# Performance work log

Hardware: AMD Instinct MI355X
Metric: run time of the kernel (lower is better)

The kernel has to match this reference:

```python
import jax, jax.numpy as jnp
import numpy as np

D_MODEL = 1024
N_HEAD = 16
D_HEAD = D_MODEL // N_HEAD
NEG = -1e9


def setup_inputs() -> dict:
    key = jax.random.key(0)
    ks = jax.random.split(key, 11)
    B, T, C = 4, 2048, D_MODEL
    s = 1.0 / np.sqrt(C)
    return {
        "q": jax.random.normal(ks[0], (B, T, C), jnp.float32),
        "k": jax.random.normal(ks[1], (B, T, C), jnp.float32),
        "v": jax.random.normal(ks[2], (B, T, C), jnp.float32),
        "w_q": jax.random.normal(ks[3], (C, C), jnp.float32) * s,
        "b_q": jnp.zeros((C,), jnp.float32),
        "w_k": jax.random.normal(ks[4], (C, C), jnp.float32) * s,
        "b_k": jnp.zeros((C,), jnp.float32),
        "w_v": jax.random.normal(ks[5], (C, C), jnp.float32) * s,
        "b_v": jnp.zeros((C,), jnp.float32),
        "w_o": jax.random.normal(ks[6], (C, C), jnp.float32) * s,
        "b_o": jnp.zeros((C,), jnp.float32),
    }


def reference(q, k, v, w_q, b_q, w_k, b_k, w_v, b_v, w_o, b_o):
    B, T, C = q.shape
    # projections; weights stored as [in, out]
    qh = (q @ w_q + b_q).reshape(B, T, N_HEAD, D_HEAD).transpose(0, 2, 1, 3)
    kh = (k @ w_k + b_k).reshape(B, T, N_HEAD, D_HEAD).transpose(0, 2, 1, 3)
    vh = (v @ w_v + b_v).reshape(B, T, N_HEAD, D_HEAD).transpose(0, 2, 1, 3)
    scores = jnp.einsum("bhqd,bhkd->bhqk", qh, kh) / jnp.sqrt(
        jnp.asarray(D_HEAD, qh.dtype))
    causal = jnp.tril(jnp.ones((T, T), dtype=bool))  # [T,T]
    scores = jnp.where(causal[None, None], scores, NEG)
    attn = jax.nn.softmax(scores, axis=-1)
    out = jnp.einsum("bhqk,bhkd->bhqd", attn, vh)
    out = out.transpose(0, 2, 1, 3).reshape(B, T, C)
    return out @ w_o + b_o
```

## Files before the change

kernel.cpp:

```cpp
#include <hip/hip_runtime.h>
#include <hip/hip_bf16.h>
#include <cstdint>
#include <cstddef>

#define DEVI static __device__ __forceinline__

typedef __attribute__((ext_vector_type(8))) short short8;
typedef __attribute__((ext_vector_type(4))) float f32x4;

typedef __attribute__((address_space(1))) const unsigned int as1c_uint;
typedef __attribute__((address_space(3))) unsigned int as3_uint;

constexpr int Bn = 4, Tn = 2048, Cn = 1024, Hn = 16, Dn = 64;
constexpr int Mtot = Bn * Tn;
#define QSCALE (0.125f * 1.44269504088896340736f)

DEVI unsigned short f2bf(float f) {
  unsigned u = __float_as_uint(f);
  u += 0x7fffu + ((u >> 16) & 1u);
  return (unsigned short)(u >> 16);
}
DEVI unsigned short f2bf_t(float f) {
  return (unsigned short)(__float_as_uint(f) >> 16);
}

DEVI void async16(const void* g, void* l) {
  __builtin_amdgcn_global_load_lds((as1c_uint*)g, (as3_uint*)l, 16, 0, 0);
}

__global__ __launch_bounds__(256) void transpose_cvt4(
    const float* __restrict__ w0, const float* __restrict__ w1,
    const float* __restrict__ w2, const float* __restrict__ w3,
    unsigned short* __restrict__ o0, unsigned short* __restrict__ o1,
    unsigned short* __restrict__ o2, unsigned short* __restrict__ o3) {
  __shared__ float tile[32][33];
  const int z = blockIdx.z;
  const float* w = z == 0 ? w0 : z == 1 ? w1 : z == 2 ? w2 : w3;
  unsigned short* wT = z == 0 ? o0 : z == 1 ? o1 : z == 2 ? o2 : o3;
  int n0 = blockIdx.x * 32, k0 = blockIdx.y * 32;
  int tx = threadIdx.x, ty = threadIdx.y;
#pragma unroll
  for (int r = 0; r < 32; r += 8)
    tile[ty + r][tx] = w[(size_t)(k0 + ty + r) * Cn + n0 + tx];
  __syncthreads();
  const int t = ty * 32 + tx;
  const int n_l = t >> 3;
  const int kq = (t & 7) * 4;
  const int n = n0 + n_l, k = k0 + kq;
  ushort4 pk;
#pragma unroll
  for (int e = 0; e < 4; ++e) ((unsigned short*)&pk)[e] = f2bf(tile[kq + e][n_l]);
  size_t idx = (size_t)((((n >> 4) * 32 + (k >> 5)) * 64 + ((k >> 3) & 3) * 16 + (n & 15))) * 8 + (k & 7);
  *(ushort4*)&wT[idx] = pk;
}

DEVI short8 xfrag(const unsigned short* Xlds, int i, int kc, int l15, int l4) {
  int row = i * 16 + l15;
  return *(const short8*)&Xlds[row * 1024 + (((kc * 4 + l4) ^ (row & 7)) * 8)];
}

template <int IB, int NJ, bool SWAP>
DEVI void proj_core(const unsigned short* __restrict__ wF,
                    const unsigned short* Xlds, int njb, int lane,
                    f32x4 (&acc)[IB][NJ]) {
  const int l15 = lane & 15, l4 = lane >> 4;
  const short8* wp = (const short8*)wF;
  short8 wfA[NJ], wfB[NJ];
#pragma unroll
  for (int j = 0; j < NJ; ++j) wfA[j] = wp[(size_t)((njb + j) * 32) * 64 + lane];
#pragma unroll 1
  for (int kc = 0; kc < 32; kc += 2) {
#pragma unroll
    for (int j = 0; j < NJ; ++j)
      wfB[j] = wp[(size_t)((njb + j) * 32 + kc + 1) * 64 + lane];
    short8 xf[IB];
#pragma unroll
    for (int i = 0; i < IB; ++i) xf[i] = xfrag(Xlds, i, kc, l15, l4);
#pragma unroll
    for (int i = 0; i < IB; ++i)
#pragma unroll
      for (int j = 0; j < NJ; ++j)
        acc[i][j] = SWAP
            ? __builtin_amdgcn_mfma_f32_16x16x32_bf16(xf[i], wfA[j], acc[i][j], 0, 0, 0)
            : __builtin_amdgcn_mfma_f32_16x16x32_bf16(wfA[j], xf[i], acc[i][j], 0, 0, 0);
    if (kc + 2 < 32) {
#pragma unroll
      for (int j = 0; j < NJ; ++j)
        wfA[j] = wp[(size_t)((njb + j) * 32 + kc + 2) * 64 + lane];
    }
#pragma unroll
    for (int i = 0; i < IB; ++i) xf[i] = xfrag(Xlds, i, kc + 1, l15, l4);
#pragma unroll
    for (int i = 0; i < IB; ++i)
#pragma unroll
      for (int j = 0; j < NJ; ++j)
        acc[i][j] = SWAP
            ? __builtin_amdgcn_mfma_f32_16x16x32_bf16(xf[i], wfB[j], acc[i][j], 0, 0, 0)
            : __builtin_amdgcn_mfma_f32_16x16x32_bf16(wfB[j], xf[i], acc[i][j], 0, 0, 0);
  }
}

DEVI void stage64_f32(const float* __restrict__ src, int m0,
                      unsigned short* Xlds, int tid) {
#pragma unroll
  for (int it = 0; it < 8; ++it) {
    int g = it * 1024 + tid;
    int row = g >> 7, slot = g & 127;
    const float4* p = (const float4*)(src + (size_t)(m0 + row) * Cn + slot * 8);
    float4 a = p[0], b = p[1];
    short8 sv;
    sv[0] = (short)f2bf(a.x); sv[1] = (short)f2bf(a.y);
    sv[2] = (short)f2bf(a.z); sv[3] = (short)f2bf(a.w);
    sv[4] = (short)f2bf(b.x); sv[5] = (short)f2bf(b.y);
    sv[6] = (short)f2bf(b.z); sv[7] = (short)f2bf(b.w);
    *(short8*)&Xlds[row * 1024 + ((slot ^ (row & 7)) * 8)] = sv;
  }
}

DEVI void stage32_bf(const unsigned short* __restrict__ src, int m0,
                     unsigned short* Xlds, int tid) {
#pragma unroll
  for (int it = 0; it < 8; ++it) {
    int s = it * 512 + tid;
    int row = s >> 7, sl = s & 127;
    async16(src + (size_t)(m0 + row) * Cn + ((sl ^ (row & 7)) * 8),
            Xlds + (size_t)(it * 512 + (tid & ~63)) * 8);
  }
}

__global__ __launch_bounds__(1024, 4) void proj_qkv(
    const float* __restrict__ xqf, const float* __restrict__ xkf,
    const float* __restrict__ xvf, const unsigned short* __restrict__ wFq,
    const unsigned short* __restrict__ wFk, const unsigned short* __restrict__ wFv,
    const float* __restrict__ bq, const float* __restrict__ bk,
    const float* __restrict__ bv, unsigned short* __restrict__ oq,
    unsigned short* __restrict__ ok, unsigned short* __restrict__ ov) {
  __shared__ unsigned short Xlds[64 * 1024];
  const int tid = threadIdx.x, lane = tid & 63, w = tid >> 6;
  const int l15 = lane & 15, l4 = lane >> 4;
  const int bid = blockIdx.x;
  const int z = bid >> 8;
  const int r = bid & 255;
  const int m0 = (r >> 1) * 64;
  const int nh = r & 1;
  const float* xz = z == 0 ? xqf : z == 1 ? xkf : xvf;
  const unsigned short* wF = z == 0 ? wFq : z == 1 ? wFk : wFv;
  const float* bias = z == 0 ? bq : z == 1 ? bk : bv;

  stage64_f32(xz, m0, Xlds, tid);
  __syncthreads();

  const f32x4 zf = {0.f, 0.f, 0.f, 0.f};
  f32x4 acc[4][2];
#pragma unroll
  for (int i = 0; i < 4; ++i)
#pragma unroll
    for (int j = 0; j < 2; ++j) acc[i][j] = zf;

  const int njb = nh * 32 + w * 2;
  if (z < 2)
    proj_core<4, 2, false>(wF, Xlds, njb, lane, acc);
  else
    proj_core<4, 2, true>(wF, Xlds, njb, lane, acc);

  const int b = m0 >> 11, t0loc = m0 & 2047;
  if (z < 2) {
    unsigned short* o = z == 0 ? oq : ok;
    const float scale = z == 0 ? QSCALE : 1.f;
#pragma unroll
    for (int j = 0; j < 2; ++j) {
      int ng = njb + j;
      int h = ng >> 2, d0 = (ng & 3) * 16 + l4 * 4;
      float4 bv4 = *(const float4*)&bias[ng * 16 + l4 * 4];
#pragma unroll
      for (int i = 0; i < 4; ++i) {
        int t = t0loc + i * 16 + l15;
        ushort4 pk;
        pk.x = f2bf((acc[i][j][0] + bv4.x) * scale);
        pk.y = f2bf((acc[i][j][1] + bv4.y) * scale);
        pk.z = f2bf((acc[i][j][2] + bv4.z) * scale);
        pk.w = f2bf((acc[i][j][3] + bv4.w) * scale);
        *(ushort4*)&o[((size_t)((b * Hn + h) * Tn + t)) * Dn + d0] = pk;
      }
    }
  } else {
#pragma unroll
    for (int j = 0; j < 2; ++j) {
      int n = (njb + j) * 16 + l15;
      int h = n >> 6, d = n & 63;
      float bvl = bias[n];
#pragma unroll
      for (int i = 0; i < 4; ++i) {
        int t0 = t0loc + i * 16 + l4 * 4;
        ushort4 pk;
        pk.x = f2bf(acc[i][j][0] + bvl);
        pk.y = f2bf(acc[i][j][1] + bvl);
        pk.z = f2bf(acc[i][j][2] + bvl);
        pk.w = f2bf(acc[i][j][3] + bvl);
        *(ushort4*)&ov[((size_t)((b * Hn + h) * Dn + d)) * Tn + t0] = pk;
      }
    }
  }
}

__global__ __launch_bounds__(512, 4) void proj_out(
    const unsigned short* __restrict__ A, const unsigned short* __restrict__ wFo,
    const float* __restrict__ bias, float* __restrict__ o) {
  __shared__ unsigned short Xlds[32 * 1024];
  const int tid = threadIdx.x, lane = tid & 63, w = tid >> 6;
  const int l15 = lane & 15, l4 = lane >> 4;
  const int bid = blockIdx.x;
  const int m0 = (bid >> 1) * 32, nh = bid & 1;

  stage32_bf(A, m0, Xlds, tid);
  __syncthreads();

  const f32x4 zf = {0.f, 0.f, 0.f, 0.f};
  f32x4 acc[2][4];
#pragma unroll
  for (int i = 0; i < 2; ++i)
#pragma unroll
    for (int j = 0; j < 4; ++j) acc[i][j] = zf;

  const int njb = nh * 32 + w * 4;
  proj_core<2, 4, false>(wFo, Xlds, njb, lane, acc);

#pragma unroll
  for (int j = 0; j < 4; ++j) {
    int ng = njb + j;
    float4 bv4 = *(const float4*)&bias[ng * 16 + l4 * 4];
#pragma unroll
    for (int i = 0; i < 2; ++i) {
      int m = m0 + i * 16 + l15;
      float4 ov4;
      ov4.x = acc[i][j][0] + bv4.x;
      ov4.y = acc[i][j][1] + bv4.y;
      ov4.z = acc[i][j][2] + bv4.z;
      ov4.w = acc[i][j][3] + bv4.w;
      *(float4*)&o[(size_t)m * Cn + ng * 16 + l4 * 4] = ov4;
    }
  }
}

__global__ __launch_bounds__(512) void attn_kernel(const unsigned short* __restrict__ qh,
                                                   const unsigned short* __restrict__ kh,
                                                   const unsigned short* __restrict__ vt,
                                                   unsigned short* __restrict__ obf) {
  __shared__ unsigned short Ks[2][64 * 64];
  __shared__ unsigned short Vs[2][64 * 64];
  __shared__ unsigned short Ps[8][16 * 72];

  const int tid = threadIdx.x, lane = tid & 63, w = tid >> 6;
  const int l15 = lane & 15, l4 = lane >> 4;
  const int swz = l15 & 7;

  const int bid = blockIdx.x;
  const int j = bid >> 3;
  const int bh = (bid & 7) * 8 + (j & 7);
  const int pair = j >> 3;
  const unsigned short* qb = qh + (size_t)bh * Tn * Dn;
  const unsigned short* kb = kh + (size_t)bh * Tn * Dn;
  const unsigned short* vb = vt + (size_t)bh * Dn * Tn;
  const int b = bh >> 4, h = bh & 15;

  const int srow = lane >> 3, sslot = (lane & 7) ^ (lane >> 3);

  const f32x4 z = {0.f, 0.f, 0.f, 0.f};
  const short ob = (short)0x3F80;
  const short8 ones = {ob, ob, ob, ob, ob, ob, ob, ob};

#pragma unroll 1
  for (int half = 0; half < 2; ++half) {
    const int qt = half == 0 ? pair : 15 - pair;
    const int q0 = qt * 128;
    const int qrow = q0 + w * 16 + l15;

    short8 qf0 = *(const short8*)(qb + (size_t)qrow * Dn + l4 * 8);
    short8 qf1 = *(const short8*)(qb + (size_t)qrow * Dn + 32 + l4 * 8);

    f32x4 o[4];
#pragma unroll
    for (int nd = 0; nd < 4; ++nd) o[nd] = z;
    f32x4 osum = z;

    const int nt = (q0 >> 6) + 2;
    const int ntw = ((q0 + w * 16 + 15) >> 6) + 1;

    {
      const unsigned short* ksrc = kb + (size_t)(w * 8 + srow) * Dn + sslot * 8;
      const unsigned short* vsrc = vb + (size_t)(w * 8 + srow) * Tn + sslot * 8;
      async16(ksrc, &Ks[0][w * 512]);
      async16(vsrc, &Vs[0][w * 512]);
    }

#pragma unroll 1
    for (int t = 0; t < nt; ++t) {
      const int cur = t & 1;
      if (t + 1 < nt) {
        const int kv1 = (t + 1) * 64;
        const unsigned short* ksrc = kb + (size_t)(kv1 + w * 8 + srow) * Dn + sslot * 8;
        const unsigned short* vsrc = vb + (size_t)(w * 8 + srow) * Tn + kv1 + sslot * 8;
        async16(ksrc, &Ks[cur ^ 1][w * 512]);
        async16(vsrc, &Vs[cur ^ 1][w * 512]);
        asm volatile("s_waitcnt vmcnt(2)" ::: "memory");
      } else {
        asm volatile("s_waitcnt vmcnt(0)" ::: "memory");
      }
      __builtin_amdgcn_s_barrier();
      __builtin_amdgcn_sched_barrier(0);

      if (t < ntw) {
        const unsigned short* Kc = &Ks[cur][0];
        const unsigned short* Vc = &Vs[cur][0];

        f32x4 s[4];
#pragma unroll
        for (int ni = 0; ni < 4; ++ni) s[ni] = z;
        __builtin_amdgcn_s_setprio(1);
#pragma unroll
        for (int ni = 0; ni < 4; ++ni) {
          const int rb = (ni * 16 + l15) * 64;
          short8 kf0 = *(const short8*)&Kc[rb + ((l4 ^ swz) * 8)];
          short8 kf1 = *(const short8*)&Kc[rb + (((4 + l4) ^ swz) * 8)];
          s[ni] = __builtin_amdgcn_mfma_f32_16x16x32_bf16(kf0, qf0, s[ni], 0, 0, 0);
          s[ni] = __builtin_amdgcn_mfma_f32_16x16x32_bf16(kf1, qf1, s[ni], 0, 0, 0);
        }
        __builtin_amdgcn_s_setprio(0);

        short8 vf[8];
#pragma unroll
        for (int nd = 0; nd < 4; ++nd) {
          const int rb = (nd * 16 + l15) * 64;
          vf[nd * 2]     = *(const short8*)&Vc[rb + ((l4 ^ swz) * 8)];
          vf[nd * 2 + 1] = *(const short8*)&Vc[rb + (((4 + l4) ^ swz) * 8)];
        }

        const int kq = qrow - t * 64;
        const bool edge = (t * 64 + 63 > q0 + w * 16);
        if (!edge) {
#pragma unroll
          for (int ni = 0; ni < 4; ++ni) {
            ushort4 pk;
#pragma unroll
            for (int r = 0; r < 4; ++r)
              ((unsigned short*)&pk)[r] = f2bf_t(__builtin_amdgcn_exp2f(s[ni][r]));
            *(ushort4*)&Ps[w][l15 * 72 + ni * 16 + l4 * 4] = pk;
          }
        } else {
#pragma unroll
          for (int ni = 0; ni < 4; ++ni) {
            ushort4 pk;
#pragma unroll
            for (int r = 0; r < 4; ++r) {
              float e = __builtin_amdgcn_exp2f(s[ni][r]);
              if ((ni * 16 + l4 * 4 + r) > kq) e = 0.f;
              ((unsigned short*)&pk)[r] = f2bf_t(e);
            }
            *(ushort4*)&Ps[w][l15 * 72 + ni * 16 + l4 * 4] = pk;
          }
        }
        asm volatile("s_waitcnt lgkmcnt(0)" ::: "memory");
        __builtin_amdgcn_sched_barrier(0);

        short8 pf0 = *(const short8*)&Ps[w][l15 * 72 + l4 * 8];
        short8 pf1 = *(const short8*)&Ps[w][l15 * 72 + 32 + l4 * 8];
        __builtin_amdgcn_s_setprio(1);
        osum = __builtin_amdgcn_mfma_f32_16x16x32_bf16(pf0, ones, osum, 0, 0, 0);
        osum = __builtin_amdgcn_mfma_f32_16x16x32_bf16(pf1, ones, osum, 0, 0, 0);
#pragma unroll
        for (int nd = 0; nd < 4; ++nd) {
          o[nd] = __builtin_amdgcn_mfma_f32_16x16x32_bf16(pf0, vf[nd * 2], o[nd], 0, 0, 0);
          o[nd] = __builtin_amdgcn_mfma_f32_16x16x32_bf16(pf1, vf[nd * 2 + 1], o[nd], 0, 0, 0);
        }
        __builtin_amdgcn_s_setprio(0);
      }

      __builtin_amdgcn_sched_barrier(0);
      __builtin_amdgcn_s_barrier();
    }

#pragma unroll
    for (int r = 0; r < 4; ++r) {
      float inv = __builtin_amdgcn_rcpf(osum[r]);
      int tq = q0 + w * 16 + l4 * 4 + r;
      size_t base = ((size_t)(b * Tn + tq)) * Cn + h * 64;
#pragma unroll
      for (int nd = 0; nd < 4; ++nd)
        obf[base + nd * 16 + l15] = f2bf(o[nd][r] * inv);
    }
  }
}

extern "C" void kernel_launch(void* const* d_in, const int* in_sizes, int n_in,
                              void* d_out, int out_size, void* d_ws, size_t ws_size,
                              hipStream_t stream) {
  const float* q   = (const float*)d_in[0];
  const float* k   = (const float*)d_in[1];
  const float* v   = (const float*)d_in[2];
  const float* w_q = (const float*)d_in[3];
  const float* b_q = (const float*)d_in[4];
  const float* w_k = (const float*)d_in[5];
  const float* b_k = (const float*)d_in[6];
  const float* w_v = (const float*)d_in[7];
  const float* b_v = (const float*)d_in[8];
  const float* w_o = (const float*)d_in[9];
  const float* b_o = (const float*)d_in[10];

  char* ws = (char*)d_ws;
  const size_t MB = 1u << 20;
  unsigned short* qhp  = (unsigned short*)(ws);
  unsigned short* khp  = (unsigned short*)(ws + 16 * MB);
  unsigned short* vtp  = (unsigned short*)(ws + 32 * MB);
  unsigned short* aout = (unsigned short*)(ws + 48 * MB);
  unsigned short* wqT  = (unsigned short*)(ws + 64 * MB);
  unsigned short* wkT  = (unsigned short*)(ws + 66 * MB);
  unsigned short* wvT  = (unsigned short*)(ws + 68 * MB);
  unsigned short* woT  = (unsigned short*)(ws + 70 * MB);

  transpose_cvt4<<<dim3(32, 32, 4), dim3(32, 8), 0, stream>>>(
      w_q, w_k, w_v, w_o, wqT, wkT, wvT, woT);

  proj_qkv<<<768, 1024, 0, stream>>>(q, k, v, wqT, wkT, wvT,
                                     b_q, b_k, b_v, qhp, khp, vtp);

  attn_kernel<<<512, 512, 0, stream>>>(qhp, khp, vtp, aout);

  proj_out<<<512, 512, 0, stream>>>(aout, woT, b_o, (float*)d_out);
}
```

Baseline: 174.2 us.

## Warp-specialize QKV projection with producer waves staging halves of X

Rewrites the QKV projection so each block handles one 64-row slice for q, k and v in sequence. Half the waves convert and stage fp32 input into a double-buffered LDS half-K tile while the other eight waves run MFMAs with wider 4x4 accumulator tiles. The grid shrinks from 768 to 256 blocks, and global fp32 loads are meant to overlap with compute. The risks are that only half the waves do math, the stage and compute phases are serialized by barriers, and 256 blocks may underfill the device.

```diff
diff --git a/kernel.cpp b/kernel.cpp
--- a/kernel.cpp
+++ b/kernel.cpp
@@ -54,6 +54,163 @@
   *(ushort4*)&wT[idx] = pk;
 }
 
+template <int NT>
+DEVI void stage_half(const float* __restrict__ src, int m0, int kh,
+                     unsigned short* Xbuf, int t) {
+#pragma unroll
+  for (int it = 0; it < 4096 / NT; ++it) {
+    int g = it * NT + t;
+    int row = g >> 6, slot = g & 63;
+    const float4* p = (const float4*)(src + (size_t)(m0 + row) * Cn + kh * 512 + slot * 8);
+    float4 a = p[0], b = p[1];
+    short8 sv;
+    sv[0] = (short)f2bf(a.x); sv[1] = (short)f2bf(a.y);
+    sv[2] = (short)f2bf(a.z); sv[3] = (short)f2bf(a.w);
+    sv[4] = (short)f2bf(b.x); sv[5] = (short)f2bf(b.y);
+    sv[6] = (short)f2bf(b.z); sv[7] = (short)f2bf(b.w);
+    *(short8*)&Xbuf[row * 512 + ((slot ^ (row & 7)) * 8)] = sv;
+  }
+}
+
+template <bool SWAP>
+DEVI void compute_half(const unsigned short* __restrict__ wF,
+                       const unsigned short* Xb, int kh, int njb, int lane,
+                       f32x4 (&acc)[4][4]) {
+  const int l15 = lane & 15, l4 = lane >> 4;
+  const short8* wp = (const short8*)wF;
+#pragma unroll
+  for (int kc = 0; kc < 16; ++kc) {
+    short8 wf[4];
+#pragma unroll
+    for (int j = 0; j < 4; ++j)
+      wf[j] = wp[(size_t)((njb + j) * 32 + kh * 16 + kc) * 64 + lane];
+#pragma unroll
+    for (int i = 0; i < 4; ++i) {
+      int row = i * 16 + l15;
+      short8 xf = *(const short8*)&Xb[row * 512 + (((kc * 4 + l4) ^ (row & 7)) * 8)];
+#pragma unroll
+      for (int j = 0; j < 4; ++j)
+        acc[i][j] = SWAP
+            ? __builtin_amdgcn_mfma_f32_16x16x32_bf16(xf, wf[j], acc[i][j], 0, 0, 0)
+            : __builtin_amdgcn_mfma_f32_16x16x32_bf16(wf[j], xf, acc[i][j], 0, 0, 0);
+    }
+  }
+}
+
+DEVI void acc_reset(f32x4 (&acc)[4][4]) {
+  const f32x4 zf = {0.f, 0.f, 0.f, 0.f};
+#pragma unroll
+  for (int i = 0; i < 4; ++i)
+#pragma unroll
+    for (int j = 0; j < 4; ++j) acc[i][j] = zf;
+}
+
+DEVI void epi_qk(const f32x4 (&acc)[4][4], const float* __restrict__ bias,
+                 unsigned short* __restrict__ o, float scale, int njb,
+                 int b, int t0loc, int l15, int l4) {
+#pragma unroll
+  for (int j = 0; j < 4; ++j) {
+    int ng = njb + j;
+    int h = ng >> 2, d0 = (ng & 3) * 16 + l4 * 4;
+    float4 bv4 = *(const float4*)&bias[ng * 16 + l4 * 4];
+#pragma unroll
+    for (int i = 0; i < 4; ++i) {
+      int t = t0loc + i * 16 + l15;
+      ushort4 pk;
+      pk.x = f2bf((acc[i][j][0] + bv4.x) * scale);
+      pk.y = f2bf((acc[i][j][1] + bv4.y) * scale);
+      pk.z = f2bf((acc[i][j][2] + bv4.z) * scale);
+      pk.w = f2bf((acc[i][j][3] + bv4.w) * scale);
+      *(ushort4*)&o[((size_t)((b * Hn + h) * Tn + t)) * Dn + d0] = pk;
+    }
+  }
+}
+
+DEVI void epi_v(const f32x4 (&acc)[4][4], const float* __restrict__ bias,
+                unsigned short* __restrict__ ov, int njb,
+                int b, int t0loc, int l15, int l4) {
+#pragma unroll
+  for (int j = 0; j < 4; ++j) {
+    int n = (njb + j) * 16 + l15;
+    int h = n >> 6, d = n & 63;
+    float bvl = bias[n];
+#pragma unroll
+    for (int i = 0; i < 4; ++i) {
+      int t0 = t0loc + i * 16 + l4 * 4;
+      ushort4 pk;
+      pk.x = f2bf(acc[i][j][0] + bvl);
+      pk.y = f2bf(acc[i][j][1] + bvl);
+      pk.z = f2bf(acc[i][j][2] + bvl);
+      pk.w = f2bf(acc[i][j][3] + bvl);
+      *(ushort4*)&ov[((size_t)((b * Hn + h) * Dn + d)) * Tn + t0] = pk;
+    }
+  }
+}
+
+__global__ __launch_bounds__(1024) void proj_qkv(
+    const float* __restrict__ xqf, const float* __restrict__ xkf,
+    const float* __restrict__ xvf, const unsigned short* __restrict__ wFq,
+    const unsigned short* __restrict__ wFk, const unsigned short* __restrict__ wFv,
+    const float* __restrict__ bq, const float* __restrict__ bk,
+    const float* __restrict__ bv, unsigned short* __restrict__ oq,
+    unsigned short* __restrict__ ok, unsigned short* __restrict__ ov) {
+  __shared__ unsigned short X[2][64 * 512];
+  const int tid = threadIdx.x, lane = tid & 63, w = tid >> 6;
+  const int l15 = lane & 15, l4 = lane >> 4;
+  const int bid = blockIdx.x;
+  const int m0 = (bid >> 1) * 64;
+  const int nh = bid & 1;
+  const int b = m0 >> 11, t0loc = m0 & 2047;
+  const bool is_stage = (w >= 8);
+  const int stid = tid - 512;
+  const int njb = nh * 32 + (w & 7) * 4;
+
+  stage_half<1024>(xqf, m0, 0, X[0], tid);
+  __syncthreads();
+
+  f32x4 acc[4][4];
+
+  if (is_stage) {
+    stage_half<512>(xqf, m0, 1, X[1], stid);
+  } else {
+    acc_reset(acc);
+    compute_half<false>(wFq, X[0], 0, njb, lane, acc);
+  }
+  __syncthreads();
+  if (is_stage) {
+    stage_half<512>(xkf, m0, 0, X[0], stid);
+  } else {
+    compute_half<false>(wFq, X[1], 1, njb, lane, acc);
+    epi_qk(acc, bq, oq, QSCALE, njb, b, t0loc, l15, l4);
+  }
+  __syncthreads();
+  if (is_stage) {
+    stage_half<512>(xkf, m0, 1, X[1], stid);
+  } else {
+    acc_reset(acc);
+    compute_half<false>(wFk, X[0], 0, njb, lane, acc);
+  }
+  __syncthreads();
+  if (is_stage) {
+    stage_half<512>(xvf, m0, 0, X[0], stid);
+  } else {
+    compute_half<false>(wFk, X[1], 1, njb, lane, acc);
+    epi_qk(acc, bk, ok, 1.f, njb, b, t0loc, l15, l4);
+  }
+  __syncthreads();
+  if (is_stage) {
+    stage_half<512>(xvf, m0, 1, X[1], stid);
+  } else {
+    acc_reset(acc);
+    compute_half<true>(wFv, X[0], 0, njb, lane, acc);
+  }
+  __syncthreads();
+  if (!is_stage) {
+    compute_half<true>(wFv, X[1], 1, njb, lane, acc);
+    epi_v(acc, bv, ov, njb, b, t0loc, l15, l4);
+  }
+}
+
 DEVI short8 xfrag(const unsigned short* Xlds, int i, int kc, int l15, int l4) {
   int row = i * 16 + l15;
   return *(const short8*)&Xlds[row * 1024 + (((kc * 4 + l4) ^ (row & 7)) * 8)];
@@ -100,23 +257,6 @@
   }
 }
 
-DEVI void stage64_f32(const float* __restrict__ src, int m0,
-                      unsigned short* Xlds, int tid) {
-#pragma unroll
-  for (int it = 0; it < 8; ++it) {
-    int g = it * 1024 + tid;
-    int row = g >> 7, slot = g & 127;
-    const float4* p = (const float4*)(src + (size_t)(m0 + row) * Cn + slot * 8);
-    float4 a = p[0], b = p[1];
-    short8 sv;
-    sv[0] = (short)f2bf(a.x); sv[1] = (short)f2bf(a.y);
-    sv[2] = (short)f2bf(a.z); sv[3] = (short)f2bf(a.w);
-    sv[4] = (short)f2bf(b.x); sv[5] = (short)f2bf(b.y);
-    sv[6] = (short)f2bf(b.z); sv[7] = (short)f2bf(b.w);
-    *(short8*)&Xlds[row * 1024 + ((slot ^ (row & 7)) * 8)] = sv;
-  }
-}
-
 DEVI void stage32_bf(const unsigned short* __restrict__ src, int m0,
                      unsigned short* Xlds, int tid) {
 #pragma unroll
@@ -125,81 +265,6 @@
     int row = s >> 7, sl = s & 127;
     async16(src + (size_t)(m0 + row) * Cn + ((sl ^ (row & 7)) * 8),
             Xlds + (size_t)(it * 512 + (tid & ~63)) * 8);
-  }
-}
-
-__global__ __launch_bounds__(1024, 4) void proj_qkv(
-    const float* __restrict__ xqf, const float* __restrict__ xkf,
-    const float* __restrict__ xvf, const unsigned short* __restrict__ wFq,
-    const unsigned short* __restrict__ wFk, const unsigned short* __restrict__ wFv,
-    const float* __restrict__ bq, const float* __restrict__ bk,
-    const float* __restrict__ bv, unsigned short* __restrict__ oq,
-    unsigned short* __restrict__ ok, unsigned short* __restrict__ ov) {
-  __shared__ unsigned short Xlds[64 * 1024];
-  const int tid = threadIdx.x, lane = tid & 63, w = tid >> 6;
-  const int l15 = lane & 15, l4 = lane >> 4;
-  const int bid = blockIdx.x;
-  const int z = bid >> 8;
-  const int r = bid & 255;
-  const int m0 = (r >> 1) * 64;
-  const int nh = r & 1;
-  const float* xz = z == 0 ? xqf : z == 1 ? xkf : xvf;
-  const unsigned short* wF = z == 0 ? wFq : z == 1 ? wFk : wFv;
-  const float* bias = z == 0 ? bq : z == 1 ? bk : bv;
-
-  stage64_f32(xz, m0, Xlds, tid);
-  __syncthreads();
-
-  const f32x4 zf = {0.f, 0.f, 0.f, 0.f};
-  f32x4 acc[4][2];
-#pragma unroll
-  for (int i = 0; i < 4; ++i)
-#pragma unroll
-    for (int j = 0; j < 2; ++j) acc[i][j] = zf;
-
-  const int njb = nh * 32 + w * 2;
-  if (z < 2)
-    proj_core<4, 2, false>(wF, Xlds, njb, lane, acc);
-  else
-    proj_core<4, 2, true>(wF, Xlds, njb, lane, acc);
-
-  const int b = m0 >> 11, t0loc = m0 & 2047;
-  if (z < 2) {
-    unsigned short* o = z == 0 ? oq : ok;
-    const float scale = z == 0 ? QSCALE : 1.f;
-#pragma unroll
-    for (int j = 0; j < 2; ++j) {
-      int ng = njb + j;
-      int h = ng >> 2, d0 = (ng & 3) * 16 + l4 * 4;
-      float4 bv4 = *(const float4*)&bias[ng * 16 + l4 * 4];
-#pragma unroll
-      for (int i = 0; i < 4; ++i) {
-        int t = t0loc + i * 16 + l15;
-        ushort4 pk;
-        pk.x = f2bf((acc[i][j][0] + bv4.x) * scale);
-        pk.y = f2bf((acc[i][j][1] + bv4.y) * scale);
-        pk.z = f2bf((acc[i][j][2] + bv4.z) * scale);
-        pk.w = f2bf((acc[i][j][3] + bv4.w) * scale);
-        *(ushort4*)&o[((size_t)((b * Hn + h) * Tn + t)) * Dn + d0] = pk;
-      }
-    }
-  } else {
-#pragma unroll
-    for (int j = 0; j < 2; ++j) {
-      int n = (njb + j) * 16 + l15;
-      int h = n >> 6, d = n & 63;
-      float bvl = bias[n];
-#pragma unroll
-      for (int i = 0; i < 4; ++i) {
-        int t0 = t0loc + i * 16 + l4 * 4;
-        ushort4 pk;
-        pk.x = f2bf(acc[i][j][0] + bvl);
-        pk.y = f2bf(acc[i][j][1] + bvl);
-        pk.z = f2bf(acc[i][j][2] + bvl);
-        pk.w = f2bf(acc[i][j][3] + bvl);
-        *(ushort4*)&ov[((size_t)((b * Hn + h) * Dn + d)) * Tn + t0] = pk;
-      }
-    }
   }
 }
 
@@ -420,7 +485,7 @@
   transpose_cvt4<<<dim3(32, 32, 4), dim3(32, 8), 0, stream>>>(
       w_q, w_k, w_v, w_o, wqT, wkT, wvT, woT);
 
-  proj_qkv<<<768, 1024, 0, stream>>>(q, k, v, wqT, wkT, wvT,
+  proj_qkv<<<256, 1024, 0, stream>>>(q, k, v, wqT, wkT, wvT,
                                      b_q, b_k, b_v, qhp, khp, vtp);
 
   attn_kernel<<<512, 512, 0, stream>>>(qhp, khp, vtp, aout);
```

Result: slower. 193.6 us (+11.1%).
